# Kernel optimization log

Hardware: AMD Instinct MI355X
Metric: run time of the kernel (lower is better)

The kernel has to match this reference:

```python
import jax, jax.numpy as jnp
import numpy as np

N = 64
H_IN = W_IN = 512
K = 9
H_OUT = H_IN - (K - 1)  # 504 (stride=1, dilation=1, no padding)
W_OUT = W_IN - (K - 1)  # 504


def setup_inputs() -> dict:
    key = jax.random.key(0)
    k1, k2, k3 = jax.random.split(key, 3)
    x = jax.random.normal(k1, (N, H_IN, W_IN), dtype=jnp.float32)
    # torch.rand -> uniform [0,1)
    weight = jax.random.uniform(k2, (H_OUT, W_OUT, K, K), dtype=jnp.float32)
    bias = jax.random.uniform(k3, (H_OUT, W_OUT), dtype=jnp.float32)
    return {"x": x, "weight": weight, "bias": bias}


def reference(x, weight, bias):
    # Locally connected 2D (no weight sharing):
    #   y[n,h,w] = sum_{i,j} x[n, h+i, w+j] * weight[h, w, i, j] + bias[h, w]
    # Equivalent to the original unfold + einsum('nklhw,hwkl->nhw'), but we
    # accumulate over the small fixed k*k taps with static slices instead of
    # materializing the huge [N,k,k,H_out,W_out] patch tensor.
    acc = jnp.zeros((x.shape[0], H_OUT, W_OUT), dtype=x.dtype)
    for i in range(K):
        for j in range(K):
            acc = acc + x[:, i:i + H_OUT, j:j + W_OUT] * weight[None, :, :, i, j]
    y = acc + bias[None, :, :]
    return jax.nn.relu(y)
```

## Files before the change

### kernel.cpp

```cpp
#include <hip/hip_runtime.h>


#define H_IN 512
#define W_IN 512
#define H_OUT 504
#define W_OUT 504
#define W_T 8
#define H_T 8
#define TROWS (H_T + 8)
#define XF (TROWS * 1024)
#define NTX 63
#define NTY 63
#define NBLK (NTX * NTY)

__device__ __forceinline__ float readlane_f(float v, int l) {
    return __int_as_float(__builtin_amdgcn_readlane(__float_as_int(v), l));
}

__launch_bounds__(512, 4)
__global__ void lc2d_kernel(const float* __restrict__ x,
                            const float* __restrict__ weight,
                            const float* __restrict__ bias,
                            float* __restrict__ out) {
    __shared__ float lds[XF];

    const int t    = threadIdx.x;
    const int lane = t & 63;
    const int wv   = t >> 6;

    int swz;
    {
        const int bid = blockIdx.x;
        const int xcd = bid & 7, i = bid >> 3;
        const int q = NBLK >> 3, r = NBLK & 7;
        swz = (xcd < r ? xcd * (q + 1)
                       : r * (q + 1) + (xcd - r) * q) + i;
    }
    const int ty = swz % NTY;
    const int tx = swz / NTY;
    const int h0 = ty * H_T;
    const int w0 = tx * W_T;

    {
        const int n  = t >> 3;
        const int c  = t & 7;
        const int wq = c & 3;
        const int rp = c >> 2;
        const float* gx = x + (size_t)n * (H_IN * W_IN)
                            + (size_t)(h0 + rp) * W_IN + w0 + wq * 4;
        float* ld = &lds[rp * 1024 + wq * 256 + ((n * 4) ^ (wq * 4))];
        #pragma unroll
        for (int rep = 0; rep < 8; ++rep) {
            const float4 v = *reinterpret_cast<const float4*>(gx + rep * 2 * W_IN);
            *reinterpret_cast<float4*>(ld + rep * 2048) = v;
        }
    }

    float wpk[18];
    {
        const float* wb = weight + ((size_t)(h0 + wv) * W_OUT + w0) * 81;
        const int qb = lane >> 4;
        const int rr = lane & 15;
        #pragma unroll
        for (int d = 0; d < 18; ++d) {
            const int q  = 4 * d + qb;
            const int k  = q / 9;
            const int tp = q - 9 * k;
            float v = 0.f;
            if (rr < 9) v = __builtin_nontemporal_load(wb + k * 81 + rr * 9 + tp);
            wpk[d] = v;
        }
    }

    __syncthreads();

    const int wvu = __builtin_amdgcn_readfirstlane(wv);
    const int h   = h0 + wvu;

    float acc[W_T];
    {
        const float* bptr = bias + (size_t)h * W_OUT + w0;
        #pragma unroll
        for (int k = 0; k < W_T; ++k) acc[k] = bptr[k];
    }

    const float* xp0 = &lds[0 * 256 + ((lane * 4) ^ 0)  + wvu * 1024];
    const float* xp1 = &lds[1 * 256 + ((lane * 4) ^ 4)  + wvu * 1024];
    const float* xp2 = &lds[2 * 256 + ((lane * 4) ^ 8)  + wvu * 1024];
    const float* xp3 = &lds[3 * 256 + ((lane * 4) ^ 12) + wvu * 1024];

    #pragma unroll 1
    for (int r = 0; r < 9; ++r) {
        float xr[16];
        {
            const float4 v0 = *reinterpret_cast<const float4*>(xp0);
            const float4 v1 = *reinterpret_cast<const float4*>(xp1);
            const float4 v2 = *reinterpret_cast<const float4*>(xp2);
            const float4 v3 = *reinterpret_cast<const float4*>(xp3);
            xr[0]  = v0.x; xr[1]  = v0.y; xr[2]  = v0.z; xr[3]  = v0.w;
            xr[4]  = v1.x; xr[5]  = v1.y; xr[6]  = v1.z; xr[7]  = v1.w;
            xr[8]  = v2.x; xr[9]  = v2.y; xr[10] = v2.z; xr[11] = v2.w;
            xr[12] = v3.x; xr[13] = v3.y; xr[14] = v3.z; xr[15] = v3.w;
        }

        const int li0 = r;
        const int li1 = r + 16;
        const int li2 = r + 32;
        const int li3 = r + 48;

        #pragma unroll
        for (int tp = 0; tp < 9; ++tp) {
            #pragma unroll
            for (int k = 0; k < W_T; ++k) {
                const int q  = k * 9 + tp;
                const int qm = q & 3;
                const int li = (qm == 0) ? li0 : (qm == 1) ? li1
                             : (qm == 2) ? li2 : li3;
                const float w = readlane_f(wpk[q >> 2], li);
                acc[k] = fmaf(w, xr[k + tp], acc[k]);
            }
        }

        xp0 += 1024; xp1 += 1024; xp2 += 1024; xp3 += 1024;
    }

    float* o = out + (size_t)lane * (H_OUT * W_OUT) + (size_t)h * W_OUT + w0;
    float4 s;
    s.x = fmaxf(acc[0], 0.f); s.y = fmaxf(acc[1], 0.f);
    s.z = fmaxf(acc[2], 0.f); s.w = fmaxf(acc[3], 0.f);
    *reinterpret_cast<float4*>(o) = s;
    s.x = fmaxf(acc[4], 0.f); s.y = fmaxf(acc[5], 0.f);
    s.z = fmaxf(acc[6], 0.f); s.w = fmaxf(acc[7], 0.f);
    *reinterpret_cast<float4*>(o + 4) = s;
}

extern "C" void kernel_launch(void* const* d_in, const int* in_sizes, int n_in,
                              void* d_out, int out_size, void* d_ws, size_t ws_size,
                              hipStream_t stream) {
    const float* x      = (const float*)d_in[0];
    const float* weight = (const float*)d_in[1];
    const float* bias   = (const float*)d_in[2];
    float* out          = (float*)d_out;

    dim3 grid(NBLK);
    dim3 block(512);
    lc2d_kernel<<<grid, block, 0, stream>>>(x, weight, bias, out);
}
```

Baseline: 305.4 us.

## Pre-transpose input to batch-innermost layout in workspace before main kernel

Adds a transpose kernel that rewrites x from [N,H,W] into [H,W,N] in the workspace, so the main kernel loads its LDS tile with contiguous float4 reads instead of strided per-batch gathers. The LDS reads become scalar per-lane loads with a simpler layout, the launch bound drops to 2 blocks per CU, and the weight readlanes are grouped ahead of the FMAs. The cost is an extra pass that reads and writes the whole input (64 MB of traffic) plus a second kernel launch.

```diff
diff --git a/kernel.cpp b/kernel.cpp
--- a/kernel.cpp
+++ b/kernel.cpp
@@ -7,7 +7,7 @@
 #define W_OUT 504
 #define W_T 8
 #define H_T 8
-#define TROWS (H_T + 8)
+#define TROWS 16
 #define XF (TROWS * 1024)
 #define NTX 63
 #define NTY 63
@@ -17,8 +17,41 @@
     return __int_as_float(__builtin_amdgcn_readlane(__float_as_int(v), l));
 }
 
-__launch_bounds__(512, 4)
-__global__ void lc2d_kernel(const float* __restrict__ x,
+__launch_bounds__(256, 4)
+__global__ void xpose_kernel(const float* __restrict__ x,
+                             float* __restrict__ xt) {
+    __shared__ float tl[64 * 68];
+    const int t  = threadIdx.x;
+    const int h  = blockIdx.x;
+    const int w0 = blockIdx.y << 6;
+
+    {
+        const int n = t >> 2, c = t & 3;
+        const float* g = x + (size_t)n * (H_IN * W_IN)
+                           + (size_t)h * W_IN + w0 + c * 16;
+        float* l = &tl[n * 68 + c * 16];
+        #pragma unroll
+        for (int j = 0; j < 4; ++j)
+            *reinterpret_cast<float4*>(l + j * 4) =
+                *reinterpret_cast<const float4*>(g + j * 4);
+    }
+    __syncthreads();
+    {
+        const int wl = t >> 2, seg = t & 3;
+        float o[16];
+        #pragma unroll
+        for (int k = 0; k < 16; ++k)
+            o[k] = tl[(seg * 16 + k) * 68 + wl];
+        float* g = xt + ((size_t)h * W_IN + w0 + wl) * 64 + seg * 16;
+        #pragma unroll
+        for (int j = 0; j < 4; ++j)
+            *reinterpret_cast<float4*>(g + j * 4) =
+                make_float4(o[4 * j], o[4 * j + 1], o[4 * j + 2], o[4 * j + 3]);
+    }
+}
+
+__launch_bounds__(512, 2)
+__global__ void lc2d_kernel(const float* __restrict__ xt,
                             const float* __restrict__ weight,
                             const float* __restrict__ bias,
                             float* __restrict__ out) {
@@ -42,18 +75,14 @@
     const int w0 = tx * W_T;
 
     {
-        const int n  = t >> 3;
-        const int c  = t & 7;
-        const int wq = c & 3;
-        const int rp = c >> 2;
-        const float* gx = x + (size_t)n * (H_IN * W_IN)
-                            + (size_t)(h0 + rp) * W_IN + w0 + wq * 4;
-        float* ld = &lds[rp * 1024 + wq * 256 + ((n * 4) ^ (wq * 4))];
+        const int row = t >> 5;
+        const int i   = t & 31;
+        const float* g = xt + ((size_t)(h0 + row) * W_IN + w0) * 64 + i * 4;
+        float* l = &lds[row * 1024 + i * 4];
         #pragma unroll
-        for (int rep = 0; rep < 8; ++rep) {
-            const float4 v = *reinterpret_cast<const float4*>(gx + rep * 2 * W_IN);
-            *reinterpret_cast<float4*>(ld + rep * 2048) = v;
-        }
+        for (int rep = 0; rep < 8; ++rep)
+            *reinterpret_cast<float4*>(l + rep * 128) =
+                *reinterpret_cast<const float4*>(g + rep * 128);
     }
 
     float wpk[18];
@@ -84,24 +113,15 @@
         for (int k = 0; k < W_T; ++k) acc[k] = bptr[k];
     }
 
-    const float* xp0 = &lds[0 * 256 + ((lane * 4) ^ 0)  + wvu * 1024];
-    const float* xp1 = &lds[1 * 256 + ((lane * 4) ^ 4)  + wvu * 1024];
-    const float* xp2 = &lds[2 * 256 + ((lane * 4) ^ 8)  + wvu * 1024];
-    const float* xp3 = &lds[3 * 256 + ((lane * 4) ^ 12) + wvu * 1024];
+    const float* xb = &lds[lane];
 
     #pragma unroll 1
     for (int r = 0; r < 9; ++r) {
+        const int rb = (wvu + r) * 1024;
         float xr[16];
-        {
-            const float4 v0 = *reinterpret_cast<const float4*>(xp0);
-            const float4 v1 = *reinterpret_cast<const float4*>(xp1);
-            const float4 v2 = *reinterpret_cast<const float4*>(xp2);
-            const float4 v3 = *reinterpret_cast<const float4*>(xp3);
-            xr[0]  = v0.x; xr[1]  = v0.y; xr[2]  = v0.z; xr[3]  = v0.w;
-            xr[4]  = v1.x; xr[5]  = v1.y; xr[6]  = v1.z; xr[7]  = v1.w;
-            xr[8]  = v2.x; xr[9]  = v2.y; xr[10] = v2.z; xr[11] = v2.w;
-            xr[12] = v3.x; xr[13] = v3.y; xr[14] = v3.z; xr[15] = v3.w;
-        }
+        #pragma unroll
+        for (int j = 0; j < 16; ++j)
+            xr[j] = xb[rb + j * 64];
 
         const int li0 = r;
         const int li1 = r + 16;
@@ -110,18 +130,19 @@
 
         #pragma unroll
         for (int tp = 0; tp < 9; ++tp) {
+            float wsv[W_T];
             #pragma unroll
             for (int k = 0; k < W_T; ++k) {
                 const int q  = k * 9 + tp;
                 const int qm = q & 3;
                 const int li = (qm == 0) ? li0 : (qm == 1) ? li1
                              : (qm == 2) ? li2 : li3;
-                const float w = readlane_f(wpk[q >> 2], li);
-                acc[k] = fmaf(w, xr[k + tp], acc[k]);
+                wsv[k] = readlane_f(wpk[q >> 2], li);
             }
+            #pragma unroll
+            for (int k = 0; k < W_T; ++k)
+                acc[k] = fmaf(wsv[k], xr[k + tp], acc[k]);
         }
-
-        xp0 += 1024; xp1 += 1024; xp2 += 1024; xp3 += 1024;
     }
 
     float* o = out + (size_t)lane * (H_OUT * W_OUT) + (size_t)h * W_OUT + w0;
@@ -141,8 +162,8 @@
     const float* weight = (const float*)d_in[1];
     const float* bias   = (const float*)d_in[2];
     float* out          = (float*)d_out;
+    float* xt           = (float*)d_ws;
 
-    dim3 grid(NBLK);
-    dim3 block(512);
-    lc2d_kernel<<<grid, block, 0, stream>>>(x, weight, bias, out);
+    xpose_kernel<<<dim3(H_IN, W_IN / 64), 256, 0, stream>>>(x, xt);
+    lc2d_kernel<<<dim3(NBLK), 512, 0, stream>>>(xt, weight, bias, out);
 }
```

Measured after the change: 309.1 us. About the same (+1.2%).
